# Optimization experiments

Hardware: AMD Instinct MI355X
Metric: run time of the kernel (lower is better)

The kernel has to match this reference:

```python
import jax, jax.numpy as jnp
import numpy as np

B, H, W, C = 4, 448, 448, 3
P = 16
G = 28            # grid = H // P
T = G * G         # 784 patches
E = 768
HD = 3072
NH = 12
DH = E // NH
L = 6
LW = 9            # local_window


def _ln(x, g, b, eps=1e-5):
    m = x.mean(-1, keepdims=True)
    v = ((x - m) ** 2).mean(-1, keepdims=True)
    return (x - m) / jnp.sqrt(v + eps) * g + b


def _mask_bias():
    # torch bool attn_mask: True = disallowed. The module sets True for LOCAL
    # neighbors (|dr|<=lw//2 and |dc|<=lw//2), so local positions are MASKED OUT.
    idx = jnp.arange(T)
    r, c = idx // G, idx % G
    local = (jnp.abs(r[:, None] - r[None, :]) <= LW // 2) & \
            (jnp.abs(c[:, None] - c[None, :]) <= LW // 2)
    return jnp.where(local, -jnp.inf, 0.0).astype(jnp.float32)  # [T, T]


def _img_to_patch(x):
    # x: [B,H,W,C] -> [B,T,C*P*P], channel-major within a patch (matches torch code)
    x = x.transpose(0, 3, 1, 2)                       # [B,C,H,W]
    x = x.reshape(B, C, G, P, G, P)
    x = x.transpose(0, 2, 4, 1, 3, 5)                 # [B,G,G,C,P,P]
    return x.reshape(B, T, C * P * P)


def _forward(x, sxr_mean, sxr_std, input_w, input_b, pos_emb,
             ln1_w, ln1_b, in_w, in_b, out_w, out_b, ln2_w, ln2_b,
             w1, b1, w2, b2, head_ln_w, head_ln_b, head_w, head_b):
    h = _img_to_patch(x) @ input_w.T + input_b        # [B,T,E]
    h = (h.reshape(B, G, G, E) + pos_emb).reshape(B, T, E)
    bias = _mask_bias()

    def block(h, prm):
        l1w, l1b, iw, ib, ow, ob, l2w, l2b, W1, B1, W2, B2 = prm
        y = _ln(h, l1w, l1b)
        qkv = y @ iw.T + ib                           # [B,T,3E]
        q, k, v = jnp.split(qkv, 3, axis=-1)
        q = q.reshape(B, T, NH, DH)
        k = k.reshape(B, T, NH, DH)
        v = v.reshape(B, T, NH, DH)
        s = jnp.einsum('bqhd,bkhd->bhqk', q, k) / jnp.sqrt(jnp.float32(DH)) + bias
        a = jax.nn.softmax(s, axis=-1)
        o = jnp.einsum('bhqk,bkhd->bqhd', a, v).reshape(B, T, E)
        h = h + o @ ow.T + ob
        y2 = _ln(h, l2w, l2b)
        m = jax.nn.gelu(y2 @ W1.T + B1, approximate=False)  # torch nn.GELU default
        h = h + m @ W2.T + B2
        return h, None

    h, _ = jax.lax.scan(block, h, (ln1_w, ln1_b, in_w, in_b, out_w, out_b,
                                   ln2_w, ln2_b, w1, b1, w2, b2))

    logits = (_ln(h, head_ln_w, head_ln_b) @ head_w.T + head_b)[..., 0]  # [B,T]
    patch_flux = jnp.clip(10.0 ** (logits * sxr_std[0] + sxr_mean[0]) - 1e-8,
                          1e-15, 1.0)
    global_flux = jnp.maximum(patch_flux.sum(axis=1, keepdims=True), 1e-15)
    return global_flux, patch_flux


def setup_inputs() -> dict:
    key = jax.random.key(0)
    ks = iter(jax.random.split(key, 16))
    def p(shape, s=0.02):
        return jax.random.normal(next(ks), shape, jnp.float32) * s
    return dict(
        x=jax.random.normal(next(ks), (B, H, W, C), jnp.float32),
        sxr_mean=jnp.array([-6.0], jnp.float32),
        sxr_std=jnp.array([1.0], jnp.float32),
        input_w=p((E, C * P * P)), input_b=jnp.zeros(E, jnp.float32),
        pos_emb=p((1, G, G, E), 1.0),
        ln1_w=jnp.ones((L, E), jnp.float32), ln1_b=jnp.zeros((L, E), jnp.float32),
        in_w=p((L, 3 * E, E)), in_b=jnp.zeros((L, 3 * E), jnp.float32),
        out_w=p((L, E, E)), out_b=jnp.zeros((L, E), jnp.float32),
        ln2_w=jnp.ones((L, E), jnp.float32), ln2_b=jnp.zeros((L, E), jnp.float32),
        w1=p((L, HD, E)), b1=jnp.zeros((L, HD), jnp.float32),
        w2=p((L, E, HD)), b2=jnp.zeros((L, E), jnp.float32),
        head_ln_w=jnp.ones(E, jnp.float32), head_ln_b=jnp.zeros(E, jnp.float32),
        head_w=p((1, E)), head_b=jnp.zeros(1, jnp.float32),
    )


def reference(x, sxr_mean, sxr_std, input_w, input_b, pos_emb,
              ln1_w, ln1_b, in_w, in_b, out_w, out_b, ln2_w, ln2_b,
              w1, b1, w2, b2, head_ln_w, head_ln_b, head_w, head_b):
    return _forward(x, sxr_mean, sxr_std, input_w, input_b, pos_emb,
                    ln1_w, ln1_b, in_w, in_b, out_w, out_b, ln2_w, ln2_b,
                    w1, b1, w2, b2, head_ln_w, head_ln_b, head_w, head_b)
```

## Files before the change

### kernel.cpp

```cpp
#include <hip/hip_runtime.h>
#include <math.h>

#define BB 4
#define TT 784
#define GG 28
#define EE 768
#define HDIM 3072
#define NHEAD 12
#define NLAYER 6
#define TTP 832

typedef short bfrag __attribute__((ext_vector_type(8)));
typedef float ffrag __attribute__((ext_vector_type(4)));

__device__ __forceinline__ unsigned short f2b(float f) {
    union { float f; unsigned u; } v; v.f = f;
    unsigned r = v.u + 0x7FFF + ((v.u >> 16) & 1);
    return (unsigned short)(r >> 16);
}

#define GLOAD_LDS16(g, l)                                                          \
    __builtin_amdgcn_global_load_lds(                                              \
        (const __attribute__((address_space(1))) void*)(g),                        \
        (__attribute__((address_space(3))) void*)(l), 16, 0, 0)

__device__ __forceinline__ void swz_bxyz(int& bx, int& by, int& bz) {
    int gx = gridDim.x, gy = gridDim.y, gz = gridDim.z;
    int nwg = gx * gy * gz;
    int orig = blockIdx.x + gx * (blockIdx.y + gy * blockIdx.z);
    int q = nwg >> 3, r = nwg & 7;
    int xc = orig & 7, li = orig >> 3;
    int wg = (xc < r ? xc * (q + 1) : r * (q + 1) + (xc - r) * q) + li;
    bx = wg % gx;
    int t = wg / gx;
    by = t % gy;
    bz = t / gy;
}

__device__ __forceinline__ float block_reduce_sum256(float v, volatile float* sb) {
    #pragma unroll
    for (int m = 1; m < 64; m <<= 1) v += __shfl_xor(v, m, 64);
    int wave = threadIdx.x >> 6;
    if ((threadIdx.x & 63) == 0) sb[wave] = v;
    __syncthreads();
    return sb[0] + sb[1] + sb[2] + sb[3];
}

__global__ __launch_bounds__(256) void cast_kernel(const float* __restrict__ s,
                                                   unsigned short* __restrict__ d, int n4) {
    int i = blockIdx.x * 256 + threadIdx.x;
    if (i >= n4) return;
    float4 v = ((const float4*)s)[i];
    ushort4 o;
    o.x = f2b(v.x); o.y = f2b(v.y); o.z = f2b(v.z); o.w = f2b(v.w);
    ((ushort4*)d)[i] = o;
}

__global__ __launch_bounds__(256) void fused_cast_kernel(const float* __restrict__ iw,
                                                         const float* __restrict__ ow,
                                                         const float* __restrict__ W1,
                                                         const float* __restrict__ W2,
                                                         unsigned short* __restrict__ dq,
                                                         unsigned short* __restrict__ doo,
                                                         unsigned short* __restrict__ d1,
                                                         unsigned short* __restrict__ d2) {
    int i = blockIdx.x * 256 + threadIdx.x;
    const float* s; unsigned short* d; int k;
    if (i < 442368)            { s = iw;  d = dq;  k = i; }
    else if (i < 589824)       { s = ow;  d = doo; k = i - 442368; }
    else if (i < 1179648)      { s = W1;  d = d1;  k = i - 589824; }
    else if (i < 1769472)      { s = W2;  d = d2;  k = i - 1179648; }
    else return;
    float4 v = ((const float4*)s)[k];
    ushort4 o;
    o.x = f2b(v.x); o.y = f2b(v.y); o.z = f2b(v.z); o.w = f2b(v.w);
    ((ushort4*)d)[k] = o;
}

__global__ __launch_bounds__(256) void patchify_kernel(const float* __restrict__ x,
                                                       unsigned short* __restrict__ P) {
    int idx = blockIdx.x * blockDim.x + threadIdx.x;
    const int total = BB * TT * EE;
    if (idx >= total) return;
    int k = idx % EE;
    int t = (idx / EE) % TT;
    int b = idx / (EE * TT);
    int c = k >> 8;
    int rem = k & 255;
    int p1 = rem >> 4;
    int p2 = rem & 15;
    int g1 = t / GG, g2 = t % GG;
    int hh = g1 * 16 + p1, ww = g2 * 16 + p2;
    P[idx] = f2b(x[((b * 448 + hh) * 448 + ww) * 3 + c]);
}

__global__ __launch_bounds__(256) void posfill_kernel(float* __restrict__ h,
                                                      const float* __restrict__ pos) {
    int idx = blockIdx.x * blockDim.x + threadIdx.x;
    const int total = BB * TT * EE;
    if (idx >= total) return;
    h[idx] = pos[idx % (TT * EE)];
}

__global__ __launch_bounds__(256) void ln_kernel(const float* __restrict__ X,
                                                 const float* __restrict__ g,
                                                 const float* __restrict__ bt,
                                                 unsigned short* __restrict__ Yb,
                                                 float* Yf) {
    __shared__ float sb1[4];
    __shared__ float sb2[4];
    int row = blockIdx.x;
    int tid = threadIdx.x;
    const float* x = X + (size_t)row * EE;
    float v0 = x[tid], v1 = x[tid + 256], v2 = x[tid + 512];
    float s = block_reduce_sum256(v0 + v1 + v2, sb1);
    float mean = s * (1.0f / 768.0f);
    float d0 = v0 - mean, d1 = v1 - mean, d2 = v2 - mean;
    __syncthreads();
    float ss = block_reduce_sum256(d0 * d0 + d1 * d1 + d2 * d2, sb2);
    float rstd = rsqrtf(ss * (1.0f / 768.0f) + 1e-5f);
    float y0 = d0 * rstd * g[tid]       + bt[tid];
    float y1 = d1 * rstd * g[tid + 256] + bt[tid + 256];
    float y2 = d2 * rstd * g[tid + 512] + bt[tid + 512];
    unsigned short* yb = Yb + (size_t)row * EE;
    yb[tid] = f2b(y0); yb[tid + 256] = f2b(y1); yb[tid + 512] = f2b(y2);
    if (Yf) {
        float* yf = Yf + (size_t)row * EE;
        yf[tid] = y0; yf[tid + 256] = y1; yf[tid + 512] = y2;
    }
}

__device__ __forceinline__ void gemm_core(const unsigned short* __restrict__ A,
                                          const unsigned short* __restrict__ W,
                                          int M, int K, int m0, int n0,
                                          int kbeg, int nk,
                                          unsigned short* As,
                                          unsigned short* Ws,
                                          ffrag (&acc)[4][4]) {
    int tid = threadIdx.x;
    int wave = tid >> 6, lane = tid & 63;
    int cl = lane & 15, qd = lane >> 4;
    int sr  = lane >> 2;
    int sbk = lane & 3;
    int ssc = (sbk ^ (sr & 3)) << 3;
    int mh = (wave & 1) << 6, nh = (wave >> 1) << 6;

    const unsigned short* Asrc0;
    const unsigned short* Asrc1;
    const unsigned short* Wsrc0;
    const unsigned short* Wsrc1;
    {
        int ar0 = m0 + (wave << 5) + sr;       if (ar0 > M - 1) ar0 = M - 1;
        int ar1 = m0 + (wave << 5) + 16 + sr;  if (ar1 > M - 1) ar1 = M - 1;
        Asrc0 = A + (size_t)ar0 * K + kbeg + ssc;
        Asrc1 = A + (size_t)ar1 * K + kbeg + ssc;
        int wr0 = n0 + (wave << 5) + sr;
        int wr1 = n0 + (wave << 5) + 16 + sr;
        Wsrc0 = W + (size_t)wr0 * K + kbeg + ssc;
        Wsrc1 = W + (size_t)wr1 * K + kbeg + ssc;
    }
    int dof0 = (wave << 10);
    int dof1 = (wave << 10) + 512;
    int fo = (qd ^ (cl & 3)) << 3;

#define STAGE32(sa, sw, kk) do {                         \
        GLOAD_LDS16(Asrc0 + (kk), (sa) + dof0);          \
        GLOAD_LDS16(Asrc1 + (kk), (sa) + dof1);          \
        GLOAD_LDS16(Wsrc0 + (kk), (sw) + dof0);          \
        GLOAD_LDS16(Wsrc1 + (kk), (sw) + dof1);          \
    } while (0)

    unsigned short *a0 = As, *a1 = As + 4096, *a2 = As + 8192;
    unsigned short *w0 = Ws, *w1 = Ws + 4096, *w2 = Ws + 8192;

    STAGE32(a0, w0, 0);
    if (nk > 1) STAGE32(a1, w1, 32);

    for (int t = 0; t < nk; ++t) {
        if (t + 2 < nk) {
            STAGE32(a2, w2, (t + 2) << 5);
            asm volatile("s_waitcnt vmcnt(8)" ::: "memory");
        } else if (t + 1 < nk) {
            asm volatile("s_waitcnt vmcnt(4)" ::: "memory");
        } else {
            asm volatile("s_waitcnt vmcnt(0)" ::: "memory");
        }
        __builtin_amdgcn_s_barrier();
        __builtin_amdgcn_sched_barrier(0);

        bfrag af[4], bf[4];
        #pragma unroll
        for (int i = 0; i < 4; i++)
            af[i] = *(const bfrag*)&a0[((mh + (i << 4) + cl) << 5) + fo];
        #pragma unroll
        for (int j = 0; j < 4; j++)
            bf[j] = *(const bfrag*)&w0[((nh + (j << 4) + cl) << 5) + fo];
        #pragma unroll
        for (int i = 0; i < 4; i++)
            #pragma unroll
            for (int j = 0; j < 4; j++)
                acc[i][j] = __builtin_amdgcn_mfma_f32_16x16x32_bf16(af[i], bf[j], acc[i][j], 0, 0, 0);

        __builtin_amdgcn_s_barrier();
        unsigned short* tp;
        tp = a0; a0 = a1; a1 = a2; a2 = tp;
        tp = w0; w0 = w1; w1 = w2; w2 = tp;
    }
#undef STAGE32
}

__global__ __launch_bounds__(256) void gemm_bf16(const unsigned short* __restrict__ A,
                                                 const unsigned short* __restrict__ W,
                                                 const float* __restrict__ bias,
                                                 const float* R, float* C,
                                                 unsigned short* Cb,
                                                 int M, int N, int K, int act) {
    __shared__ __align__(16) unsigned short As[3 * 4096];
    __shared__ __align__(16) unsigned short Ws[3 * 4096];
    int bx, by, bz;
    swz_bxyz(bx, by, bz);
    int m0 = by << 7, n0 = bx << 7;

    ffrag acc[4][4] = {};
    gemm_core(A, W, M, K, m0, n0, 0, K >> 5, As, Ws, acc);

    int tid = threadIdx.x;
    int wave = tid >> 6, lane = tid & 63;
    int cl = lane & 15, qd = lane >> 4;
    int mh = (wave & 1) << 6, nh = (wave >> 1) << 6;

    #pragma unroll
    for (int j = 0; j < 4; j++) {
        int col = n0 + nh + (j << 4) + cl;
        float bv = bias[col];
        #pragma unroll
        for (int i = 0; i < 4; i++) {
            int row0 = m0 + mh + (i << 4) + (qd << 2);
            #pragma unroll
            for (int r = 0; r < 4; r++) {
                int row = row0 + r;
                if (row < M) {
                    float v = acc[i][j][r] + bv;
                    if (R) v += R[(size_t)row * N + col];
                    if (act) v = 0.5f * v * (1.0f + erff(v * 0.70710678118654752f));
                    if (C)  C[(size_t)row * N + col] = v;
                    if (Cb) Cb[(size_t)row * N + col] = f2b(v);
                }
            }
        }
    }
}

__global__ __launch_bounds__(256) void gemm_qkv(const unsigned short* __restrict__ A,
                                                const unsigned short* __restrict__ W,
                                                const float* __restrict__ bias,
                                                unsigned short* __restrict__ Q,
                                                unsigned short* __restrict__ Kd,
                                                unsigned short* __restrict__ vT,
                                                int M, int N, int K) {
    __shared__ __align__(16) unsigned short As[3 * 4096];
    __shared__ __align__(16) unsigned short Ws[3 * 4096];
    int bx, by, bz;
    swz_bxyz(bx, by, bz);
    int m0 = by << 7, n0 = bx << 7;

    ffrag acc[4][4] = {};
    gemm_core(A, W, M, K, m0, n0, 0, K >> 5, As, Ws, acc);

    int tid = threadIdx.x;
    int wave = tid >> 6, lane = tid & 63;
    int cl = lane & 15, qd = lane >> 4;
    int mh = (wave & 1) << 6, nh = (wave >> 1) << 6;

    int ncb = n0 + nh;
    if (ncb < 1536) {
        unsigned short* dst = (ncb < 768) ? Q : Kd;
        int cb = (ncb < 768) ? 0 : 768;
        #pragma unroll
        for (int j = 0; j < 4; j++) {
            int col = ncb + (j << 4) + cl;
            float bv = bias[col];
            #pragma unroll
            for (int i = 0; i < 4; i++) {
                int row0 = m0 + mh + (i << 4) + (qd << 2);
                #pragma unroll
                for (int r = 0; r < 4; r++) {
                    int row = row0 + r;
                    if (row < M)
                        dst[(size_t)row * EE + col - cb] = f2b(acc[i][j][r] + bv);
                }
            }
        }
    } else {
        int hh = (ncb - 1536) >> 6;
        #pragma unroll
        for (int i = 0; i < 4; i++) {
            int row0 = m0 + mh + (i << 4) + (qd << 2);
            #pragma unroll
            for (int r = 0; r < 4; r++) {
                int row = row0 + r;
                if (row < M) {
                    int b = row / TT;
                    int t = row - b * TT;
                    size_t vbase = ((size_t)(b * NHEAD + hh) * 64) * TTP + t;
                    #pragma unroll
                    for (int j = 0; j < 4; j++) {
                        int col = ncb + (j << 4) + cl;
                        vT[vbase + (size_t)((j << 4) + cl) * TTP] =
                            f2b(acc[i][j][r] + bias[col]);
                    }
                }
            }
        }
    }
}

__global__ __launch_bounds__(256) void gemm_bf16_sk(const unsigned short* __restrict__ A,
                                                    const unsigned short* __restrict__ W,
                                                    const float* __restrict__ bias,
                                                    float* C,
                                                    int M, int N, int K, int KC) {
    __shared__ __align__(16) unsigned short As[3 * 4096];
    __shared__ __align__(16) unsigned short Ws[3 * 4096];
    int bx, by, bz;
    swz_bxyz(bx, by, bz);
    int m0 = by << 7, n0 = bx << 7;
    int z = bz;
    int kbeg = z * KC;
    int kc2 = (kbeg + KC > K) ? (K - kbeg) : KC;

    ffrag acc[4][4] = {};
    gemm_core(A, W, M, K, m0, n0, kbeg, kc2 >> 5, As, Ws, acc);

    int tid = threadIdx.x;
    int wave = tid >> 6, lane = tid & 63;
    int cl = lane & 15, qd = lane >> 4;
    int mh = (wave & 1) << 6, nh = (wave >> 1) << 6;

    #pragma unroll
    for (int j = 0; j < 4; j++) {
        int col = n0 + nh + (j << 4) + cl;
        float bv = (z == 0) ? bias[col] : 0.0f;
        #pragma unroll
        for (int i = 0; i < 4; i++) {
            int row0 = m0 + mh + (i << 4) + (qd << 2);
            #pragma unroll
            for (int r = 0; r < 4; r++) {
                int row = row0 + r;
                if (row < M)
                    unsafeAtomicAdd(&C[(size_t)row * N + col], acc[i][j][r] + bv);
            }
        }
    }
}

#define LP 72
#define SCL2 0.18033688011112042f
__global__ __launch_bounds__(256) void attn_kernel(const unsigned short* __restrict__ Qg,
                                                   const unsigned short* __restrict__ Kg,
                                                   const unsigned short* __restrict__ vT,
                                                   unsigned short* __restrict__ O) {
    __shared__ unsigned short Ks[64 * LP];
    __shared__ unsigned short Vt[64 * LP];
    __shared__ unsigned short Pb[64 * LP];
    int tid = threadIdx.x;
    int wave = tid >> 6, lane = tid & 63;
    int cl = lane & 15, qd = lane >> 4;
    int bh = blockIdx.y;
    int b = bh / NHEAD, hh = bh % NHEAD;
    int q0 = blockIdx.x * 64;
    int qw = q0 + wave * 16;

    int qrow = qw + cl;
    if (qrow > TT - 1) qrow = TT - 1;
    const unsigned short* qb = Qg + (size_t)(b * TT + qrow) * EE + hh * 64;
    bfrag qf0 = *(const bfrag*)(qb + (qd << 3));
    bfrag qf1 = *(const bfrag*)(qb + 32 + (qd << 3));

    ffrag o_acc[4] = {};
    float m_run[4], l_run[4];
    int qg_[4], qr_[4], qc_[4];
    #pragma unroll
    for (int r = 0; r < 4; r++) {
        qg_[r] = qw + (qd << 2) + r;
        qr_[r] = qg_[r] / GG;
        qc_[r] = qg_[r] % GG;
        m_run[r] = -1e30f; l_run[r] = 0.0f;
    }

    int kr[4], kc[4];
    #pragma unroll
    for (int j = 0; j < 4; j++) {
        int kg = j * 16 + cl;
        kr[j] = kg / GG; kc[j] = kg % GG;
    }

    const unsigned short* kbase = Kg + (size_t)b * TT * EE + hh * 64;
    const unsigned short* vbase = vT + (size_t)(b * NHEAD + hh) * 64 * TTP;
    int srow = tid >> 3;
    int scol = (tid & 7) << 3;

    for (int k0 = 0; k0 < 832; k0 += 64) {
        __syncthreads();
        #pragma unroll
        for (int it = 0; it < 2; it++) {
            int row = it * 32 + srow;
            int tok = k0 + row; if (tok > TT - 1) tok = TT - 1;
            *(bfrag*)&Ks[row * LP + scol] =
                *(const bfrag*)(kbase + (size_t)tok * EE + scol);
            *(bfrag*)&Vt[row * LP + scol] =
                *(const bfrag*)(vbase + (size_t)row * TTP + k0 + scol);
        }
        __syncthreads();

        ffrag sv[4];
        #pragma unroll
        for (int j = 0; j < 4; j++) {
            bfrag kf0 = *(const bfrag*)&Ks[(j * 16 + cl) * LP + (qd << 3)];
            bfrag kf1 = *(const bfrag*)&Ks[(j * 16 + cl) * LP + 32 + (qd << 3)];
            ffrag z = {0.f, 0.f, 0.f, 0.f};
            z = __builtin_amdgcn_mfma_f32_16x16x32_bf16(qf0, kf0, z, 0, 0, 0);
            z = __builtin_amdgcn_mfma_f32_16x16x32_bf16(qf1, kf1, z, 0, 0, 0);
            sv[j] = z;
        }

        #pragma unroll
        for (int j = 0; j < 4; j++) {
            #pragma unroll
            for (int r = 0; r < 4; r++) {
                bool masked = (kr[j] > 27) ||
                              (abs(qr_[r] - kr[j]) <= 4 && abs(qc_[r] - kc[j]) <= 4);
                if (masked) sv[j][r] = -3.0e38f;
            }
        }

        #pragma unroll
        for (int r = 0; r < 4; r++) {
            float mx = fmaxf(fmaxf(sv[0][r], sv[1][r]), fmaxf(sv[2][r], sv[3][r]));
            mx = fmaxf(mx, __shfl_xor(mx, 1, 64));
            mx = fmaxf(mx, __shfl_xor(mx, 2, 64));
            mx = fmaxf(mx, __shfl_xor(mx, 4, 64));
            mx = fmaxf(mx, __shfl_xor(mx, 8, 64));
            float m_new = fmaxf(m_run[r], mx);
            float alpha = exp2f((m_run[r] - m_new) * SCL2);
            float p0 = exp2f((sv[0][r] - m_new) * SCL2);
            float p1 = exp2f((sv[1][r] - m_new) * SCL2);
            float p2 = exp2f((sv[2][r] - m_new) * SCL2);
            float p3 = exp2f((sv[3][r] - m_new) * SCL2);
            float rs = (p0 + p1) + (p2 + p3);
            rs += __shfl_xor(rs, 1, 64);
            rs += __shfl_xor(rs, 2, 64);
            rs += __shfl_xor(rs, 4, 64);
            rs += __shfl_xor(rs, 8, 64);
            l_run[r] = l_run[r] * alpha + rs;
            m_run[r] = m_new;
            #pragma unroll
            for (int t = 0; t < 4; t++) o_acc[t][r] *= alpha;
            int prow = (wave * 16 + (qd << 2) + r) * LP;
            Pb[prow + 0 * 16 + cl] = f2b(p0);
            Pb[prow + 1 * 16 + cl] = f2b(p1);
            Pb[prow + 2 * 16 + cl] = f2b(p2);
            Pb[prow + 3 * 16 + cl] = f2b(p3);
        }
        asm volatile("s_waitcnt lgkmcnt(0)" ::: "memory");

        bfrag pf0 = *(const bfrag*)&Pb[(wave * 16 + cl) * LP + (qd << 3)];
        bfrag pf1 = *(const bfrag*)&Pb[(wave * 16 + cl) * LP + 32 + (qd << 3)];
        #pragma unroll
        for (int t = 0; t < 4; t++) {
            bfrag vf0 = *(const bfrag*)&Vt[(t * 16 + cl) * LP + (qd << 3)];
            bfrag vf1 = *(const bfrag*)&Vt[(t * 16 + cl) * LP + 32 + (qd << 3)];
            o_acc[t] = __builtin_amdgcn_mfma_f32_16x16x32_bf16(pf0, vf0, o_acc[t], 0, 0, 0);
            o_acc[t] = __builtin_amdgcn_mfma_f32_16x16x32_bf16(pf1, vf1, o_acc[t], 0, 0, 0);
        }

        #pragma unroll
        for (int j = 0; j < 4; j++) {
            kc[j] += 8; kr[j] += 2;
            if (kc[j] >= GG) { kc[j] -= GG; kr[j] += 1; }
        }
    }

    #pragma unroll
    for (int r = 0; r < 4; r++) {
        if (qg_[r] < TT) {
            float inv = 1.0f / fmaxf(l_run[r], 1e-30f);
            #pragma unroll
            for (int t = 0; t < 4; t++)
                O[(size_t)(b * TT + qg_[r]) * EE + hh * 64 + t * 16 + cl] =
                    f2b(o_acc[t][r] * inv);
        }
    }
}

__global__ __launch_bounds__(256) void head_kernel(const float* __restrict__ Y,
                                                   const float* __restrict__ hw,
                                                   const float* __restrict__ hb,
                                                   const float* __restrict__ mean_,
                                                   const float* __restrict__ std_,
                                                   float* __restrict__ out) {
    __shared__ float sb[4];
    int row = blockIdx.x;
    int tid = threadIdx.x;
    const float* y = Y + (size_t)row * EE;
    float v = y[tid] * hw[tid] + y[tid + 256] * hw[tid + 256] + y[tid + 512] * hw[tid + 512];
    v = block_reduce_sum256(v, sb);
    if (tid == 0) {
        float logit = v + hb[0];
        float z = logit * std_[0] + mean_[0];
        float f = expf(z * 2.302585092994046f) - 1e-8f;
        f = fminf(fmaxf(f, 1e-15f), 1.0f);
        out[4 + row] = f;
    }
}

__global__ __launch_bounds__(256) void flux_sum_kernel(float* __restrict__ out) {
    __shared__ float sb[4];
    int b = blockIdx.x;
    int tid = threadIdx.x;
    const float* pf = out + 4 + (size_t)b * TT;
    float v = pf[tid] + pf[tid + 256] + pf[tid + 512];
    if (tid < TT - 768) v += pf[tid + 768];
    v = block_reduce_sum256(v, sb);
    if (tid == 0) out[b] = fmaxf(v, 1e-15f);
}

extern "C" void kernel_launch(void* const* d_in, const int* in_sizes, int n_in,
                              void* d_out, int out_size, void* d_ws, size_t ws_size,
                              hipStream_t stream) {
    const float* x        = (const float*)d_in[0];
    const float* sxr_mean = (const float*)d_in[1];
    const float* sxr_std  = (const float*)d_in[2];
    const float* input_w  = (const float*)d_in[3];
    const float* input_b  = (const float*)d_in[4];
    const float* pos_emb  = (const float*)d_in[5];
    const float* ln1_w    = (const float*)d_in[6];
    const float* ln1_b    = (const float*)d_in[7];
    const float* in_w     = (const float*)d_in[8];
    const float* in_b     = (const float*)d_in[9];
    const float* out_w    = (const float*)d_in[10];
    const float* out_b    = (const float*)d_in[11];
    const float* ln2_w    = (const float*)d_in[12];
    const float* ln2_b    = (const float*)d_in[13];
    const float* w1       = (const float*)d_in[14];
    const float* b1       = (const float*)d_in[15];
    const float* w2       = (const float*)d_in[16];
    const float* b2       = (const float*)d_in[17];
    const float* head_ln_w = (const float*)d_in[18];
    const float* head_ln_b = (const float*)d_in[19];
    const float* head_w   = (const float*)d_in[20];
    const float* head_b   = (const float*)d_in[21];
    float* out = (float*)d_out;

    const size_t NROW = (size_t)BB * TT;
    const size_t NE   = NROW * EE;

    float* h   = (float*)d_ws;
    float* y32 = h + NE;
    unsigned short* q_b   = (unsigned short*)(y32 + NE);
    unsigned short* k_b   = q_b + NE;
    unsigned short* vT_b  = k_b + NE;
    unsigned short* y_b   = vT_b + (size_t)BB * NHEAD * 64 * TTP;
    unsigned short* o_b   = y_b + NE;
    unsigned short* mlp_b = o_b + NE;
    unsigned short* wq_b  = mlp_b + NROW * HDIM;
    unsigned short* wo_b  = wq_b + (size_t)3 * EE * EE;
    unsigned short* w1_b  = wo_b + (size_t)EE * EE;
    unsigned short* w2_b  = w1_b + (size_t)HDIM * EE;

    const int tot = BB * TT * EE;
    const int GY = (int)((NROW + 127) / 128);

    patchify_kernel<<<(tot + 255) / 256, 256, 0, stream>>>(x, mlp_b);
    cast_kernel<<<(EE * EE / 4 + 255) / 256, 256, 0, stream>>>(input_w, wo_b, EE * EE / 4);
    posfill_kernel<<<(tot + 255) / 256, 256, 0, stream>>>(h, pos_emb);
    gemm_bf16_sk<<<dim3(EE / 128, GY, 4), 256, 0, stream>>>(
        mlp_b, wo_b, input_b, h, (int)NROW, EE, EE, 192);

    for (int l = 0; l < NLAYER; l++) {
        fused_cast_kernel<<<6912, 256, 0, stream>>>(
            in_w + (size_t)l * 3 * EE * EE, out_w + (size_t)l * EE * EE,
            w1 + (size_t)l * HDIM * EE, w2 + (size_t)l * EE * HDIM,
            wq_b, wo_b, w1_b, w2_b);

        ln_kernel<<<(int)NROW, 256, 0, stream>>>(h, ln1_w + l * EE, ln1_b + l * EE, y_b, nullptr);
        gemm_qkv<<<dim3(3 * EE / 128, GY), 256, 0, stream>>>(
            y_b, wq_b, in_b + (size_t)l * 3 * EE, q_b, k_b, vT_b,
            (int)NROW, 3 * EE, EE);
        attn_kernel<<<dim3(13, BB * NHEAD), 256, 0, stream>>>(q_b, k_b, vT_b, o_b);
        gemm_bf16_sk<<<dim3(EE / 128, GY, 4), 256, 0, stream>>>(
            o_b, wo_b, out_b + (size_t)l * EE, h, (int)NROW, EE, EE, 192);
        ln_kernel<<<(int)NROW, 256, 0, stream>>>(h, ln2_w + l * EE, ln2_b + l * EE, y_b, nullptr);
        gemm_bf16<<<dim3(HDIM / 128, GY), 256, 0, stream>>>(
            y_b, w1_b, b1 + (size_t)l * HDIM, nullptr, nullptr, mlp_b,
            (int)NROW, HDIM, EE, 1);
        gemm_bf16_sk<<<dim3(EE / 128, GY, 4), 256, 0, stream>>>(
            mlp_b, w2_b, b2 + (size_t)l * EE, h, (int)NROW, EE, HDIM, 768);
    }

    ln_kernel<<<(int)NROW, 256, 0, stream>>>(h, head_ln_w, head_ln_b, y_b, y32);
    head_kernel<<<(int)NROW, 256, 0, stream>>>(y32, head_w, head_b, sxr_mean, sxr_std, out);
    flux_sum_kernel<<<BB, 256, 0, stream>>>(out);
}
```

Measured before the change: 1.688 ms.

## Rework attention: register-prefetch K/V, bitmask table, MFMA row-sum, swizzled P

The attention kernel now prefetches the next K/V tile into registers while computing on the current one. It replaces the per-element geometric mask math with lookups into a precomputed 64-bit mask table. The softmax denominator is folded into the PV MFMA through an extra ones-row V tile, which removes the shuffle reductions. P writes to LDS are XOR-swizzled to cut bank conflicts, exp/rcp use raw hardware instructions, and the block index is swizzled. Costs are extra registers, an extra MFMA per tile, a small setup kernel, and less precise exp/rcp.

```diff
diff --git a/kernel.cpp b/kernel.cpp
--- a/kernel.cpp
+++ b/kernel.cpp
@@ -17,6 +17,13 @@
     union { float f; unsigned u; } v; v.f = f;
     unsigned r = v.u + 0x7FFF + ((v.u >> 16) & 1);
     return (unsigned short)(r >> 16);
+}
+
+__device__ __forceinline__ float fexp2(float x) {
+    float r; asm("v_exp_f32 %0, %1" : "=v"(r) : "v"(x)); return r;
+}
+__device__ __forceinline__ float frcp(float x) {
+    float r; asm("v_rcp_f32 %0, %1" : "=v"(r) : "v"(x)); return r;
 }
 
 #define GLOAD_LDS16(g, l)                                                          \
@@ -102,6 +109,25 @@
     h[idx] = pos[idx % (TT * EE)];
 }
 
+__global__ __launch_bounds__(256) void mask_build_kernel(unsigned long long* __restrict__ mt) {
+    int idx = blockIdx.x * 256 + threadIdx.x;
+    if (idx >= TT * 13) return;
+    int row = idx / 13, t = idx % 13;
+    int qr = row / GG, qc = row % GG;
+    unsigned long long bits = 0;
+    for (int i = 0; i < 64; i++) {
+        int k = t * 64 + i;
+        bool m;
+        if (k >= TT) m = true;
+        else {
+            int kr2 = k / GG, kc2 = k % GG;
+            m = (abs(qr - kr2) <= 4) && (abs(qc - kc2) <= 4);
+        }
+        if (m) bits |= (1ull << i);
+    }
+    mt[idx] = bits;
+}
+
 __global__ __launch_bounds__(256) void ln_kernel(const float* __restrict__ X,
                                                  const float* __restrict__ g,
                                                  const float* __restrict__ bt,
@@ -359,17 +385,23 @@
 __global__ __launch_bounds__(256) void attn_kernel(const unsigned short* __restrict__ Qg,
                                                    const unsigned short* __restrict__ Kg,
                                                    const unsigned short* __restrict__ vT,
+                                                   const unsigned long long* __restrict__ mtab,
                                                    unsigned short* __restrict__ O) {
     __shared__ unsigned short Ks[64 * LP];
-    __shared__ unsigned short Vt[64 * LP];
+    __shared__ unsigned short Vt[80 * LP];
     __shared__ unsigned short Pb[64 * LP];
     int tid = threadIdx.x;
     int wave = tid >> 6, lane = tid & 63;
     int cl = lane & 15, qd = lane >> 4;
-    int bh = blockIdx.y;
+    int bx, by, bz;
+    swz_bxyz(bx, by, bz);
+    int bh = by;
     int b = bh / NHEAD, hh = bh % NHEAD;
-    int q0 = blockIdx.x * 64;
+    int q0 = bx * 64;
     int qw = q0 + wave * 16;
+
+    for (int i = tid; i < 16 * LP; i += 256)
+        Vt[64 * LP + i] = (i < LP) ? (unsigned short)0x3F80 : (unsigned short)0;
 
     int qrow = qw + cl;
     if (qrow > TT - 1) qrow = TT - 1;
@@ -377,41 +409,59 @@
     bfrag qf0 = *(const bfrag*)(qb + (qd << 3));
     bfrag qf1 = *(const bfrag*)(qb + 32 + (qd << 3));
 
-    ffrag o_acc[4] = {};
-    float m_run[4], l_run[4];
-    int qg_[4], qr_[4], qc_[4];
+    ffrag o_acc[5] = {};
+    float m_run[4];
+    int qg_[4], qm_[4];
     #pragma unroll
     for (int r = 0; r < 4; r++) {
         qg_[r] = qw + (qd << 2) + r;
-        qr_[r] = qg_[r] / GG;
-        qc_[r] = qg_[r] % GG;
-        m_run[r] = -1e30f; l_run[r] = 0.0f;
-    }
-
-    int kr[4], kc[4];
-    #pragma unroll
-    for (int j = 0; j < 4; j++) {
-        int kg = j * 16 + cl;
-        kr[j] = kg / GG; kc[j] = kg % GG;
+        qm_[r] = qg_[r] > TT - 1 ? TT - 1 : qg_[r];
+        m_run[r] = -1e30f;
     }
 
     const unsigned short* kbase = Kg + (size_t)b * TT * EE + hh * 64;
     const unsigned short* vbase = vT + (size_t)(b * NHEAD + hh) * 64 * TTP;
     int srow = tid >> 3;
     int scol = (tid & 7) << 3;
+    int r0 = srow, r1 = 32 + srow;
+    const unsigned short* vp0 = vbase + (size_t)r0 * TTP + scol;
+    const unsigned short* vp1 = vbase + (size_t)r1 * TTP + scol;
+
+    bfrag kreg0 = *(const bfrag*)(kbase + (size_t)r0 * EE + scol);
+    bfrag kreg1 = *(const bfrag*)(kbase + (size_t)r1 * EE + scol);
+    bfrag vreg0 = *(const bfrag*)vp0;
+    bfrag vreg1 = *(const bfrag*)vp1;
+
+    int rot = (cl >> 2) & 3;
+    int pread0 = (wave * 16 + cl) * LP + ((((qd >> 1)    ) ^ rot) << 4) + ((qd & 1) << 3);
+    int pread1 = (wave * 16 + cl) * LP + (((2 + (qd >> 1)) ^ rot) << 4) + ((qd & 1) << 3);
 
     for (int k0 = 0; k0 < 832; k0 += 64) {
         __syncthreads();
-        #pragma unroll
-        for (int it = 0; it < 2; it++) {
-            int row = it * 32 + srow;
-            int tok = k0 + row; if (tok > TT - 1) tok = TT - 1;
-            *(bfrag*)&Ks[row * LP + scol] =
-                *(const bfrag*)(kbase + (size_t)tok * EE + scol);
-            *(bfrag*)&Vt[row * LP + scol] =
-                *(const bfrag*)(vbase + (size_t)row * TTP + k0 + scol);
+        *(bfrag*)&Ks[r0 * LP + scol] = kreg0;
+        *(bfrag*)&Ks[r1 * LP + scol] = kreg1;
+        *(bfrag*)&Vt[r0 * LP + scol] = vreg0;
+        *(bfrag*)&Vt[r1 * LP + scol] = vreg1;
+
+        int tix = k0 >> 6;
+        unsigned mlo[4], mhi[4];
+        #pragma unroll
+        for (int r = 0; r < 4; r++) {
+            unsigned long long mb = mtab[qm_[r] * 13 + tix];
+            mlo[r] = (unsigned)mb;
+            mhi[r] = (unsigned)(mb >> 32);
         }
         __syncthreads();
+
+        if (k0 + 64 < 832) {
+            int kn = k0 + 64;
+            int t0 = kn + r0; if (t0 > TT - 1) t0 = TT - 1;
+            int t1 = kn + r1; if (t1 > TT - 1) t1 = TT - 1;
+            kreg0 = *(const bfrag*)(kbase + (size_t)t0 * EE + scol);
+            kreg1 = *(const bfrag*)(kbase + (size_t)t1 * EE + scol);
+            vreg0 = *(const bfrag*)(vp0 + kn);
+            vreg1 = *(const bfrag*)(vp1 + kn);
+        }
 
         ffrag sv[4];
         #pragma unroll
@@ -428,9 +478,8 @@
         for (int j = 0; j < 4; j++) {
             #pragma unroll
             for (int r = 0; r < 4; r++) {
-                bool masked = (kr[j] > 27) ||
-                              (abs(qr_[r] - kr[j]) <= 4 && abs(qc_[r] - kc[j]) <= 4);
-                if (masked) sv[j][r] = -3.0e38f;
+                unsigned sel = (j < 2) ? mlo[r] : mhi[r];
+                if ((sel >> (((j & 1) << 4) + cl)) & 1) sv[j][r] = -3.0e38f;
             }
         }
 
@@ -442,49 +491,38 @@
             mx = fmaxf(mx, __shfl_xor(mx, 4, 64));
             mx = fmaxf(mx, __shfl_xor(mx, 8, 64));
             float m_new = fmaxf(m_run[r], mx);
-            float alpha = exp2f((m_run[r] - m_new) * SCL2);
-            float p0 = exp2f((sv[0][r] - m_new) * SCL2);
-            float p1 = exp2f((sv[1][r] - m_new) * SCL2);
-            float p2 = exp2f((sv[2][r] - m_new) * SCL2);
-            float p3 = exp2f((sv[3][r] - m_new) * SCL2);
-            float rs = (p0 + p1) + (p2 + p3);
-            rs += __shfl_xor(rs, 1, 64);
-            rs += __shfl_xor(rs, 2, 64);
-            rs += __shfl_xor(rs, 4, 64);
-            rs += __shfl_xor(rs, 8, 64);
-            l_run[r] = l_run[r] * alpha + rs;
+            float alpha = fexp2((m_run[r] - m_new) * SCL2);
+            float p0 = fexp2((sv[0][r] - m_new) * SCL2);
+            float p1 = fexp2((sv[1][r] - m_new) * SCL2);
+            float p2 = fexp2((sv[2][r] - m_new) * SCL2);
+            float p3 = fexp2((sv[3][r] - m_new) * SCL2);
             m_run[r] = m_new;
             #pragma unroll
-            for (int t = 0; t < 4; t++) o_acc[t][r] *= alpha;
+            for (int t = 0; t < 5; t++) o_acc[t][r] *= alpha;
             int prow = (wave * 16 + (qd << 2) + r) * LP;
-            Pb[prow + 0 * 16 + cl] = f2b(p0);
-            Pb[prow + 1 * 16 + cl] = f2b(p1);
-            Pb[prow + 2 * 16 + cl] = f2b(p2);
-            Pb[prow + 3 * 16 + cl] = f2b(p3);
+            Pb[prow + ((0 ^ qd) << 4) + cl] = f2b(p0);
+            Pb[prow + ((1 ^ qd) << 4) + cl] = f2b(p1);
+            Pb[prow + ((2 ^ qd) << 4) + cl] = f2b(p2);
+            Pb[prow + ((3 ^ qd) << 4) + cl] = f2b(p3);
         }
         asm volatile("s_waitcnt lgkmcnt(0)" ::: "memory");
 
-        bfrag pf0 = *(const bfrag*)&Pb[(wave * 16 + cl) * LP + (qd << 3)];
-        bfrag pf1 = *(const bfrag*)&Pb[(wave * 16 + cl) * LP + 32 + (qd << 3)];
-        #pragma unroll
-        for (int t = 0; t < 4; t++) {
+        bfrag pf0 = *(const bfrag*)&Pb[pread0];
+        bfrag pf1 = *(const bfrag*)&Pb[pread1];
+        #pragma unroll
+        for (int t = 0; t < 5; t++) {
             bfrag vf0 = *(const bfrag*)&Vt[(t * 16 + cl) * LP + (qd << 3)];
             bfrag vf1 = *(const bfrag*)&Vt[(t * 16 + cl) * LP + 32 + (qd << 3)];
             o_acc[t] = __builtin_amdgcn_mfma_f32_16x16x32_bf16(pf0, vf0, o_acc[t], 0, 0, 0);
             o_acc[t] = __builtin_amdgcn_mfma_f32_16x16x32_bf16(pf1, vf1, o_acc[t], 0, 0, 0);
         }
-
-        #pragma unroll
-        for (int j = 0; j < 4; j++) {
-            kc[j] += 8; kr[j] += 2;
-            if (kc[j] >= GG) { kc[j] -= GG; kr[j] += 1; }
-        }
     }
 
     #pragma unroll
     for (int r = 0; r < 4; r++) {
+        float l = __shfl(o_acc[4][r], lane & 48, 64);
+        float inv = frcp(fmaxf(l, 1e-30f));
         if (qg_[r] < TT) {
-            float inv = 1.0f / fmaxf(l_run[r], 1e-30f);
             #pragma unroll
             for (int t = 0; t < 4; t++)
                 O[(size_t)(b * TT + qg_[r]) * EE + hh * 64 + t * 16 + cl] =
@@ -567,6 +605,7 @@
     unsigned short* wo_b  = wq_b + (size_t)3 * EE * EE;
     unsigned short* w1_b  = wo_b + (size_t)EE * EE;
     unsigned short* w2_b  = w1_b + (size_t)HDIM * EE;
+    unsigned long long* mtab = (unsigned long long*)(w2_b + (size_t)EE * HDIM);
 
     const int tot = BB * TT * EE;
     const int GY = (int)((NROW + 127) / 128);
@@ -574,6 +613,7 @@
     patchify_kernel<<<(tot + 255) / 256, 256, 0, stream>>>(x, mlp_b);
     cast_kernel<<<(EE * EE / 4 + 255) / 256, 256, 0, stream>>>(input_w, wo_b, EE * EE / 4);
     posfill_kernel<<<(tot + 255) / 256, 256, 0, stream>>>(h, pos_emb);
+    mask_build_kernel<<<(TT * 13 + 255) / 256, 256, 0, stream>>>(mtab);
     gemm_bf16_sk<<<dim3(EE / 128, GY, 4), 256, 0, stream>>>(
         mlp_b, wo_b, input_b, h, (int)NROW, EE, EE, 192);
 
@@ -587,7 +627,7 @@
         gemm_qkv<<<dim3(3 * EE / 128, GY), 256, 0, stream>>>(
             y_b, wq_b, in_b + (size_t)l * 3 * EE, q_b, k_b, vT_b,
             (int)NROW, 3 * EE, EE);
-        attn_kernel<<<dim3(13, BB * NHEAD), 256, 0, stream>>>(q_b, k_b, vT_b, o_b);
+        attn_kernel<<<dim3(13, BB * NHEAD), 256, 0, stream>>>(q_b, k_b, vT_b, mtab, o_b);
         gemm_bf16_sk<<<dim3(EE / 128, GY, 4), 256, 0, stream>>>(
             o_b, wo_b, out_b + (size_t)l * EE, h, (int)NROW, EE, EE, 192);
         ln_kernel<<<(int)NROW, 256, 0, stream>>>(h, ln2_w + l * EE, ln2_b + l * EE, y_b, nullptr);
```

After: 1.583 ms. -6.2%, faster.
